# Kernel optimization log

Hardware: AMD Instinct MI355X
Metric: run time of the kernel (lower is better)

## Reference

```python
import jax, jax.numpy as jnp
import numpy as np

B, T, D, H = 8, 128, 768, 768  # batch, num tokens (actual==virtual), dim, hidden_dim
LN_EPS = 1e-5


def setup_inputs() -> dict:
    key = jax.random.key(0)
    ks = jax.random.split(key, 7)
    s1 = 1.0 / np.sqrt(D)  # torch nn.Linear init scale (uniform bound)
    s2 = 1.0 / np.sqrt(H)
    return {
        "x": jax.random.normal(ks[0], (B, T, D), dtype=jnp.float32),
        "gamma": jnp.ones((T, D), dtype=jnp.float32),
        "beta": jnp.zeros((T, D), dtype=jnp.float32),
        "W1": jax.random.uniform(ks[1], (T, D, H), minval=-s1, maxval=s1, dtype=jnp.float32),
        "b1": jax.random.uniform(ks[2], (T, H), minval=-s1, maxval=s1, dtype=jnp.float32),
        "W2": jax.random.uniform(ks[3], (T, H, D), minval=-s2, maxval=s2, dtype=jnp.float32),
        "b2": jax.random.uniform(ks[4], (T, D), minval=-s2, maxval=s2, dtype=jnp.float32),
    }


def reference(x, gamma, beta, W1, b1, W2, b2):
    # Per-token FeedForward with distinct weights per token position, fully batched
    # (equivalent to the per-token Python loop in the torch module, with
    # num_actual_tokens == num_virtual_tokens so no repeat happens).
    mu = jnp.mean(x, axis=-1, keepdims=True)
    var = jnp.mean(jnp.square(x - mu), axis=-1, keepdims=True)
    xn = (x - mu) * jax.lax.rsqrt(var + LN_EPS)
    xn = xn * gamma[None] + beta[None]                      # [B,T,D]
    h = jnp.einsum('btd,tdh->bth', xn, W1) + b1[None]       # [B,T,H]
    h = jax.nn.gelu(h, approximate=False)                   # torch nn.GELU default (erf)
    out = jnp.einsum('bth,thd->btd', h, W2) + b2[None]      # [B,T,D]
    return out + x  # residual
```

## Files before the change

kernel.cpp:

```cpp
#include <hip/hip_runtime.h>
#include <math.h>

#define TB 8
#define TT 128
#define TD 768
#define TH 768
#define LN_EPS 1e-5f

__global__ __launch_bounds__(256) void ff1_kernel(
    const float* __restrict__ x,
    const float* __restrict__ gamma,
    const float* __restrict__ beta,
    const float* __restrict__ W1,
    const float* __restrict__ b1,
    float* __restrict__ hbuf) {
  __shared__ float st[TB][TD];
  __shared__ float red[4][8][128];
  const int tid = threadIdx.x;
  const int w = tid >> 6, lane = tid & 63;
  const int half = lane >> 5, l32 = lane & 31;
  const int t = blockIdx.x / 6, slice = blockIdx.x % 6;

  {
    const int b = w * 2 + half;
    const float* xr = x + ((size_t)b * TT + t) * TD;
    float4 v[6];
    float s = 0.f, ss = 0.f;
#pragma unroll
    for (int i = 0; i < 6; ++i) {
      v[i] = *(const float4*)(xr + i * 128 + l32 * 4);
      s += v[i].x + v[i].y + v[i].z + v[i].w;
      ss += v[i].x * v[i].x + v[i].y * v[i].y + v[i].z * v[i].z + v[i].w * v[i].w;
    }
#pragma unroll
    for (int off = 16; off; off >>= 1) {
      s  += __shfl_xor(s, off, 64);
      ss += __shfl_xor(ss, off, 64);
    }
    const float mu   = s * (1.f / TD);
    const float var  = ss * (1.f / TD) - mu * mu;
    const float rstd = rsqrtf(var + LN_EPS);
#pragma unroll
    for (int i = 0; i < 6; ++i) {
      const int d = i * 128 + l32 * 4;
      const float4 g  = *(const float4*)(gamma + (size_t)t * TD + d);
      const float4 be = *(const float4*)(beta  + (size_t)t * TD + d);
      float4 o;
      o.x = (v[i].x - mu) * rstd * g.x + be.x;
      o.y = (v[i].y - mu) * rstd * g.y + be.y;
      o.z = (v[i].z - mu) * rstd * g.z + be.z;
      o.w = (v[i].w - mu) * rstd * g.w + be.w;
      *(float4*)&st[b][d] = o;
    }
  }
  __syncthreads();

  const int cg = l32 * 4;
  const int c = slice * 128 + cg;
  const int r0 = w * 192 + half * 96;
  const float* wp = W1 + ((size_t)t * TD + r0) * TH + c;

  float acc[8][4];
#pragma unroll
  for (int b = 0; b < 8; ++b)
#pragma unroll
    for (int j = 0; j < 4; ++j) acc[b][j] = 0.f;

#pragma unroll 2
  for (int dd = 0; dd < 96; dd += 4) {
    float4 wv[4];
#pragma unroll
    for (int k = 0; k < 4; ++k) wv[k] = *(const float4*)(wp + k * TH);
    wp += 4 * TH;
    float4 xq[8];
#pragma unroll
    for (int b = 0; b < 8; ++b) xq[b] = *(const float4*)&st[b][r0 + dd];
#pragma unroll
    for (int k = 0; k < 4; ++k)
#pragma unroll
      for (int b = 0; b < 8; ++b) {
        const float xv = ((const float*)&xq[b])[k];
        acc[b][0] = fmaf(xv, wv[k].x, acc[b][0]);
        acc[b][1] = fmaf(xv, wv[k].y, acc[b][1]);
        acc[b][2] = fmaf(xv, wv[k].z, acc[b][2]);
        acc[b][3] = fmaf(xv, wv[k].w, acc[b][3]);
      }
  }

#pragma unroll
  for (int b = 0; b < 8; ++b)
#pragma unroll
    for (int j = 0; j < 4; ++j)
      acc[b][j] += __shfl_xor(acc[b][j], 32, 64);

  if (lane < 32) {
#pragma unroll
    for (int b = 0; b < 8; ++b)
      *(float4*)&red[w][b][cg] =
          make_float4(acc[b][0], acc[b][1], acc[b][2], acc[b][3]);
  }
  __syncthreads();

  {
    const int b = tid >> 5;
    const int colq = (tid & 31) * 4;
    const int cc = slice * 128 + colq;
    const float4 bias = *(const float4*)(b1 + (size_t)t * TH + cc);
    float4 o;
    float* po = (float*)&o;
    const float* pb = (const float*)&bias;
#pragma unroll
    for (int k = 0; k < 4; ++k) {
      float vv = red[0][b][colq + k] + red[1][b][colq + k] +
                 red[2][b][colq + k] + red[3][b][colq + k] + pb[k];
      po[k] = 0.5f * vv * (1.f + erff(vv * 0.7071067811865476f));
    }
    *(float4*)(hbuf + ((size_t)t * TB + b) * TH + cc) = o;
  }
}

__global__ __launch_bounds__(256) void ff2_kernel(
    const float* __restrict__ hbuf,
    const float* __restrict__ W2,
    const float* __restrict__ b2,
    const float* __restrict__ x,
    float* __restrict__ out) {
  __shared__ float st[TB][TH];
  __shared__ float red[4][8][128];
  const int tid = threadIdx.x;
  const int w = tid >> 6, lane = tid & 63;
  const int half = lane >> 5, l32 = lane & 31;
  const int t = blockIdx.x / 6, slice = blockIdx.x % 6;

  {
    const float4* src = (const float4*)(hbuf + (size_t)t * TB * TH);
    float4* dst = (float4*)&st[0][0];
#pragma unroll
    for (int i = 0; i < 6; ++i) dst[tid + i * 256] = src[tid + i * 256];
  }
  __syncthreads();

  const int cg = l32 * 4;
  const int c = slice * 128 + cg;
  const int r0 = w * 192 + half * 96;
  const float* wp = W2 + ((size_t)t * TH + r0) * TD + c;

  float acc[8][4];
#pragma unroll
  for (int b = 0; b < 8; ++b)
#pragma unroll
    for (int j = 0; j < 4; ++j) acc[b][j] = 0.f;

#pragma unroll 2
  for (int dd = 0; dd < 96; dd += 4) {
    float4 wv[4];
#pragma unroll
    for (int k = 0; k < 4; ++k) wv[k] = *(const float4*)(wp + k * TD);
    wp += 4 * TD;
    float4 hq[8];
#pragma unroll
    for (int b = 0; b < 8; ++b) hq[b] = *(const float4*)&st[b][r0 + dd];
#pragma unroll
    for (int k = 0; k < 4; ++k)
#pragma unroll
      for (int b = 0; b < 8; ++b) {
        const float hv = ((const float*)&hq[b])[k];
        acc[b][0] = fmaf(hv, wv[k].x, acc[b][0]);
        acc[b][1] = fmaf(hv, wv[k].y, acc[b][1]);
        acc[b][2] = fmaf(hv, wv[k].z, acc[b][2]);
        acc[b][3] = fmaf(hv, wv[k].w, acc[b][3]);
      }
  }

#pragma unroll
  for (int b = 0; b < 8; ++b)
#pragma unroll
    for (int j = 0; j < 4; ++j)
      acc[b][j] += __shfl_xor(acc[b][j], 32, 64);

  if (lane < 32) {
#pragma unroll
    for (int b = 0; b < 8; ++b)
      *(float4*)&red[w][b][cg] =
          make_float4(acc[b][0], acc[b][1], acc[b][2], acc[b][3]);
  }
  __syncthreads();

  {
    const int b = tid >> 5;
    const int colq = (tid & 31) * 4;
    const int cc = slice * 128 + colq;
    const size_t off = ((size_t)b * TT + t) * TD + cc;
    const float4 bias = *(const float4*)(b2 + (size_t)t * TD + cc);
    const float4 xres = *(const float4*)(x + off);
    float4 o;
    float* po = (float*)&o;
    const float* pb = (const float*)&bias;
    const float* px = (const float*)&xres;
#pragma unroll
    for (int k = 0; k < 4; ++k)
      po[k] = red[0][b][colq + k] + red[1][b][colq + k] +
              red[2][b][colq + k] + red[3][b][colq + k] + pb[k] + px[k];
    *(float4*)(out + off) = o;
  }
}

extern "C" void kernel_launch(void* const* d_in, const int* in_sizes, int n_in,
                              void* d_out, int out_size, void* d_ws, size_t ws_size,
                              hipStream_t stream) {
  const float* x     = (const float*)d_in[0];
  const float* gamma = (const float*)d_in[1];
  const float* beta  = (const float*)d_in[2];
  const float* W1    = (const float*)d_in[3];
  const float* b1    = (const float*)d_in[4];
  const float* W2    = (const float*)d_in[5];
  const float* b2    = (const float*)d_in[6];
  float* out = (float*)d_out;

  float* hbuf = (float*)d_ws;

  ff1_kernel<<<TT * 6, 256, 0, stream>>>(x, gamma, beta, W1, b1, hbuf);
  ff2_kernel<<<TT * 6, 256, 0, stream>>>(hbuf, W2, b2, x, out);
}
```

Measured before the change: 115.6 us.

## Fuse both FFN stages into one kernel with per-token atomic handoff

Merges the two GEMM kernels into one. The six slice blocks of a token write their GELU outputs to a workspace buffer, bump a per-token atomic counter, then spin until all six have arrived before running the second GEMM. The first rows of W1 and then W2 are prefetched into registers early, so the load latency overlaps with layernorm and with the counter wait. This removes one kernel launch boundary and the tail gap between stages. It adds a memset launch, spin-wait cost and register pressure, and relies on all 768 blocks being co-resident (launch bounds 256,3) to avoid deadlock.

```diff
diff --git a/kernel.cpp b/kernel.cpp
--- a/kernel.cpp
+++ b/kernel.cpp
@@ -7,19 +7,49 @@
 #define TH 768
 #define LN_EPS 1e-5f
 
-__global__ __launch_bounds__(256) void ff1_kernel(
+#define BODY4(WV, ROW)                                                \
+  {                                                                   \
+    float4 xq[8];                                                     \
+    _Pragma("unroll") for (int b = 0; b < 8; ++b)                     \
+        xq[b] = *(const float4*)&st[b][(ROW)];                        \
+    _Pragma("unroll") for (int k = 0; k < 4; ++k) {                   \
+      _Pragma("unroll") for (int b = 0; b < 8; ++b) {                 \
+        const float xv = ((const float*)&xq[b])[k];                   \
+        acc[b][0] = fmaf(xv, (WV)[k].x, acc[b][0]);                   \
+        acc[b][1] = fmaf(xv, (WV)[k].y, acc[b][1]);                   \
+        acc[b][2] = fmaf(xv, (WV)[k].z, acc[b][2]);                   \
+        acc[b][3] = fmaf(xv, (WV)[k].w, acc[b][3]);                   \
+      }                                                               \
+    }                                                                 \
+  }
+
+__global__ __launch_bounds__(256, 3) void fused_ff_kernel(
     const float* __restrict__ x,
     const float* __restrict__ gamma,
     const float* __restrict__ beta,
     const float* __restrict__ W1,
     const float* __restrict__ b1,
-    float* __restrict__ hbuf) {
+    const float* __restrict__ W2,
+    const float* __restrict__ b2,
+    float* __restrict__ hbuf,
+    int* __restrict__ cnt,
+    float* __restrict__ outp) {
   __shared__ float st[TB][TD];
   __shared__ float red[4][8][128];
   const int tid = threadIdx.x;
   const int w = tid >> 6, lane = tid & 63;
   const int half = lane >> 5, l32 = lane & 31;
   const int t = blockIdx.x / 6, slice = blockIdx.x % 6;
+  const int cg = l32 * 4;
+  const int c = slice * 128 + cg;
+  const int r0 = w * 192 + half * 96;
+
+  const float* wp1 = W1 + ((size_t)t * TD + r0) * TH + c;
+  float4 pA[4], pB[4];
+#pragma unroll
+  for (int k = 0; k < 4; ++k) pA[k] = *(const float4*)(wp1 + k * TH);
+#pragma unroll
+  for (int k = 0; k < 4; ++k) pB[k] = *(const float4*)(wp1 + (4 + k) * TH);
 
   {
     const int b = w * 2 + half;
@@ -30,7 +60,8 @@
     for (int i = 0; i < 6; ++i) {
       v[i] = *(const float4*)(xr + i * 128 + l32 * 4);
       s += v[i].x + v[i].y + v[i].z + v[i].w;
-      ss += v[i].x * v[i].x + v[i].y * v[i].y + v[i].z * v[i].z + v[i].w * v[i].w;
+      ss += v[i].x * v[i].x + v[i].y * v[i].y + v[i].z * v[i].z +
+            v[i].w * v[i].w;
     }
 #pragma unroll
     for (int off = 16; off; off >>= 1) {
@@ -55,36 +86,24 @@
   }
   __syncthreads();
 
-  const int cg = l32 * 4;
-  const int c = slice * 128 + cg;
-  const int r0 = w * 192 + half * 96;
-  const float* wp = W1 + ((size_t)t * TD + r0) * TH + c;
-
   float acc[8][4];
 #pragma unroll
   for (int b = 0; b < 8; ++b)
 #pragma unroll
     for (int j = 0; j < 4; ++j) acc[b][j] = 0.f;
 
+  BODY4(pA, r0);
+  BODY4(pB, r0 + 4);
+  {
+    const float* wp = wp1 + 8 * TH;
 #pragma unroll 2
-  for (int dd = 0; dd < 96; dd += 4) {
-    float4 wv[4];
-#pragma unroll
-    for (int k = 0; k < 4; ++k) wv[k] = *(const float4*)(wp + k * TH);
-    wp += 4 * TH;
-    float4 xq[8];
-#pragma unroll
-    for (int b = 0; b < 8; ++b) xq[b] = *(const float4*)&st[b][r0 + dd];
-#pragma unroll
-    for (int k = 0; k < 4; ++k)
-#pragma unroll
-      for (int b = 0; b < 8; ++b) {
-        const float xv = ((const float*)&xq[b])[k];
-        acc[b][0] = fmaf(xv, wv[k].x, acc[b][0]);
-        acc[b][1] = fmaf(xv, wv[k].y, acc[b][1]);
-        acc[b][2] = fmaf(xv, wv[k].z, acc[b][2]);
-        acc[b][3] = fmaf(xv, wv[k].w, acc[b][3]);
-      }
+    for (int dd = 8; dd < 96; dd += 4) {
+      float4 wv[4];
+#pragma unroll
+      for (int k = 0; k < 4; ++k) wv[k] = *(const float4*)(wp + k * TH);
+      wp += 4 * TH;
+      BODY4(wv, r0 + dd);
+    }
   }
 
 #pragma unroll
@@ -92,7 +111,6 @@
 #pragma unroll
     for (int j = 0; j < 4; ++j)
       acc[b][j] += __shfl_xor(acc[b][j], 32, 64);
-
   if (lane < 32) {
 #pragma unroll
     for (int b = 0; b < 8; ++b)
@@ -117,20 +135,24 @@
     }
     *(float4*)(hbuf + ((size_t)t * TB + b) * TH + cc) = o;
   }
-}
-
-__global__ __launch_bounds__(256) void ff2_kernel(
-    const float* __restrict__ hbuf,
-    const float* __restrict__ W2,
-    const float* __restrict__ b2,
-    const float* __restrict__ x,
-    float* __restrict__ out) {
-  __shared__ float st[TB][TH];
-  __shared__ float red[4][8][128];
-  const int tid = threadIdx.x;
-  const int w = tid >> 6, lane = tid & 63;
-  const int half = lane >> 5, l32 = lane & 31;
-  const int t = blockIdx.x / 6, slice = blockIdx.x % 6;
+  __syncthreads();
+
+  if (tid == 0)
+    __hip_atomic_fetch_add(cnt + t, 1, __ATOMIC_RELEASE,
+                           __HIP_MEMORY_SCOPE_AGENT);
+
+  const float* wp2 = W2 + ((size_t)t * TH + r0) * TD + c;
+#pragma unroll
+  for (int k = 0; k < 4; ++k) pA[k] = *(const float4*)(wp2 + k * TD);
+#pragma unroll
+  for (int k = 0; k < 4; ++k) pB[k] = *(const float4*)(wp2 + (4 + k) * TD);
+
+  if (tid == 0) {
+    while (__hip_atomic_load(cnt + t, __ATOMIC_ACQUIRE,
+                             __HIP_MEMORY_SCOPE_AGENT) < 6)
+      __builtin_amdgcn_s_sleep(2);
+  }
+  __syncthreads();
 
   {
     const float4* src = (const float4*)(hbuf + (size_t)t * TB * TH);
@@ -140,36 +162,23 @@
   }
   __syncthreads();
 
-  const int cg = l32 * 4;
-  const int c = slice * 128 + cg;
-  const int r0 = w * 192 + half * 96;
-  const float* wp = W2 + ((size_t)t * TH + r0) * TD + c;
-
-  float acc[8][4];
 #pragma unroll
   for (int b = 0; b < 8; ++b)
 #pragma unroll
     for (int j = 0; j < 4; ++j) acc[b][j] = 0.f;
 
+  BODY4(pA, r0);
+  BODY4(pB, r0 + 4);
+  {
+    const float* wp = wp2 + 8 * TD;
 #pragma unroll 2
-  for (int dd = 0; dd < 96; dd += 4) {
-    float4 wv[4];
-#pragma unroll
-    for (int k = 0; k < 4; ++k) wv[k] = *(const float4*)(wp + k * TD);
-    wp += 4 * TD;
-    float4 hq[8];
-#pragma unroll
-    for (int b = 0; b < 8; ++b) hq[b] = *(const float4*)&st[b][r0 + dd];
-#pragma unroll
-    for (int k = 0; k < 4; ++k)
-#pragma unroll
-      for (int b = 0; b < 8; ++b) {
-        const float hv = ((const float*)&hq[b])[k];
-        acc[b][0] = fmaf(hv, wv[k].x, acc[b][0]);
-        acc[b][1] = fmaf(hv, wv[k].y, acc[b][1]);
-        acc[b][2] = fmaf(hv, wv[k].z, acc[b][2]);
-        acc[b][3] = fmaf(hv, wv[k].w, acc[b][3]);
-      }
+    for (int dd = 8; dd < 96; dd += 4) {
+      float4 wv[4];
+#pragma unroll
+      for (int k = 0; k < 4; ++k) wv[k] = *(const float4*)(wp + k * TD);
+      wp += 4 * TD;
+      BODY4(wv, r0 + dd);
+    }
   }
 
 #pragma unroll
@@ -177,7 +186,6 @@
 #pragma unroll
     for (int j = 0; j < 4; ++j)
       acc[b][j] += __shfl_xor(acc[b][j], 32, 64);
-
   if (lane < 32) {
 #pragma unroll
     for (int b = 0; b < 8; ++b)
@@ -201,7 +209,7 @@
     for (int k = 0; k < 4; ++k)
       po[k] = red[0][b][colq + k] + red[1][b][colq + k] +
               red[2][b][colq + k] + red[3][b][colq + k] + pb[k] + px[k];
-    *(float4*)(out + off) = o;
+    *(float4*)(outp + off) = o;
   }
 }
 
@@ -218,7 +226,9 @@
   float* out = (float*)d_out;
 
   float* hbuf = (float*)d_ws;
-
-  ff1_kernel<<<TT * 6, 256, 0, stream>>>(x, gamma, beta, W1, b1, hbuf);
-  ff2_kernel<<<TT * 6, 256, 0, stream>>>(hbuf, W2, b2, x, out);
+  int* cnt = (int*)((char*)d_ws + (size_t)TT * TB * TH * sizeof(float));
+
+  hipMemsetAsync(cnt, 0, TT * sizeof(int), stream);
+  fused_ff_kernel<<<TT * 6, 256, 0, stream>>>(x, gamma, beta, W1, b1, W2, b2,
+                                              hbuf, cnt, out);
 }
```

Result: slower. 164.4 us (+42.2%).

## Split into LN, row-chunked double-buffered GEMMs with partial sums, and reduce kernel

Applied to the files above, without the earlier changes.

Replaces the two fused kernels with four: a standalone LayerNorm kernel, two GEMM kernels where each block owns a 128-row K-chunk of the per-token weight matrix and streams it through double-buffered shared memory, and a final reduction kernel. Each GEMM block writes partial sums for all 768 outputs, and the next stage sums the six partials, then adds bias and applies GELU or the residual. The aim is fully coalesced contiguous weight streaming with register-prefetch overlap. In exchange it adds more launches and significant workspace traffic for partials, and falls back to the old path when the workspace is too small.

```diff
diff --git a/kernel.cpp b/kernel.cpp
--- a/kernel.cpp
+++ b/kernel.cpp
@@ -7,25 +7,214 @@
 #define TH 768
 #define LN_EPS 1e-5f
 
-__global__ __launch_bounds__(256) void ff1_kernel(
+
+__global__ __launch_bounds__(256) void ln_kernel(
     const float* __restrict__ x,
     const float* __restrict__ gamma,
     const float* __restrict__ beta,
-    const float* __restrict__ W1,
-    const float* __restrict__ b1,
-    float* __restrict__ hbuf) {
+    float* __restrict__ xn) {
+  const int w = threadIdx.x >> 6, lane = threadIdx.x & 63;
+  const int r = blockIdx.x * 4 + w;
+  const int t = r & (TT - 1);
+  const int b = r >> 7;
+  const float* xr = x + (size_t)r * TD;
+
+  float v[12];
+  float s = 0.f, ss = 0.f;
+#pragma unroll
+  for (int i = 0; i < 3; ++i) {
+    float4 f = *(const float4*)(xr + i * 256 + lane * 4);
+    v[i * 4 + 0] = f.x; v[i * 4 + 1] = f.y;
+    v[i * 4 + 2] = f.z; v[i * 4 + 3] = f.w;
+    s += f.x + f.y + f.z + f.w;
+    ss += f.x * f.x + f.y * f.y + f.z * f.z + f.w * f.w;
+  }
+#pragma unroll
+  for (int off = 32; off; off >>= 1) {
+    s  += __shfl_down(s, off, 64);
+    ss += __shfl_down(ss, off, 64);
+  }
+  s = __shfl(s, 0, 64); ss = __shfl(ss, 0, 64);
+  const float mu   = s * (1.f / TD);
+  const float var  = ss * (1.f / TD) - mu * mu;
+  const float rstd = rsqrtf(var + LN_EPS);
+
+#pragma unroll
+  for (int i = 0; i < 3; ++i) {
+    const int d = i * 256 + lane * 4;
+    float4 g  = *(const float4*)(gamma + (size_t)t * TD + d);
+    float4 be = *(const float4*)(beta  + (size_t)t * TD + d);
+    float4 o;
+    o.x = (v[i * 4 + 0] - mu) * rstd * g.x + be.x;
+    o.y = (v[i * 4 + 1] - mu) * rstd * g.y + be.y;
+    o.z = (v[i * 4 + 2] - mu) * rstd * g.z + be.z;
+    o.w = (v[i * 4 + 3] - mu) * rstd * g.w + be.w;
+    *(float4*)(xn + ((size_t)t * TB + b) * TD + d) = o;
+  }
+}
+
+template <int IS_G2>
+__global__ __launch_bounds__(256, 3) void gemm_kernel(
+    const float* __restrict__ act_src,
+    const float* __restrict__ W,
+    const float* __restrict__ bias,
+    float* __restrict__ pout) {
+  __shared__ float wt[2][8][768];
+  __shared__ float as[TB][128];
+  const int tid = threadIdx.x;
+  const int t = blockIdx.x / 6, chunk = blockIdx.x % 6;
+  const int c0 = tid * 3;
+
+  const float* wbase = W + ((size_t)t * 768 + chunk * 128) * 768;
+
+  float4 rstage[6];
+#pragma unroll
+  for (int k = 0; k < 6; ++k)
+    rstage[k] = *(const float4*)(wbase + (tid + k * 256) * 4);
+
+  {
+    const int b = tid >> 5, q = (tid & 31) * 4;
+    if (IS_G2) {
+      float4 sum;
+      {
+        const float* p = act_src + ((size_t)(t * 6 + 0) * TB + b) * 768 +
+                         chunk * 128 + q;
+        sum = *(const float4*)p;
+      }
+#pragma unroll
+      for (int c = 1; c < 6; ++c) {
+        const float* p = act_src + ((size_t)(t * 6 + c) * TB + b) * 768 +
+                         chunk * 128 + q;
+        const float4 v = *(const float4*)p;
+        sum.x += v.x; sum.y += v.y; sum.z += v.z; sum.w += v.w;
+      }
+      const float4 bv = *(const float4*)(bias + (size_t)t * TH + chunk * 128 + q);
+      float4 o;
+      o.x = sum.x + bv.x; o.y = sum.y + bv.y;
+      o.z = sum.z + bv.z; o.w = sum.w + bv.w;
+      float* po = (float*)&o;
+#pragma unroll
+      for (int k = 0; k < 4; ++k)
+        po[k] = 0.5f * po[k] * (1.f + erff(po[k] * 0.7071067811865476f));
+      *(float4*)&as[b][q] = o;
+    } else {
+      *(float4*)&as[b][q] =
+          *(const float4*)(act_src + ((size_t)t * TB + b) * TD + chunk * 128 + q);
+    }
+  }
+
+#pragma unroll
+  for (int k = 0; k < 6; ++k)
+    *(float4*)&wt[0][0][(tid + k * 256) * 4] = rstage[k];
+  __syncthreads();
+
+  float acc[8][3];
+#pragma unroll
+  for (int b = 0; b < 8; ++b)
+#pragma unroll
+    for (int j = 0; j < 3; ++j) acc[b][j] = 0.f;
+
+#pragma unroll 1
+  for (int tile = 0; tile < 16; ++tile) {
+    const int buf = tile & 1;
+    if (tile < 15) {
+      const float* src = wbase + (size_t)(tile + 1) * 8 * 768;
+#pragma unroll
+      for (int k = 0; k < 6; ++k)
+        rstage[k] = *(const float4*)(src + (tid + k * 256) * 4);
+    }
+    float wr[8][3];
+#pragma unroll
+    for (int r = 0; r < 8; ++r)
+#pragma unroll
+      for (int j = 0; j < 3; ++j) wr[r][j] = wt[buf][r][c0 + j];
+#pragma unroll
+    for (int b = 0; b < 8; ++b) {
+      float xa[8];
+      *(float4*)&xa[0] = *(const float4*)&as[b][tile * 8];
+      *(float4*)&xa[4] = *(const float4*)&as[b][tile * 8 + 4];
+#pragma unroll
+      for (int r = 0; r < 8; ++r) {
+        acc[b][0] = fmaf(xa[r], wr[r][0], acc[b][0]);
+        acc[b][1] = fmaf(xa[r], wr[r][1], acc[b][1]);
+        acc[b][2] = fmaf(xa[r], wr[r][2], acc[b][2]);
+      }
+    }
+    if (tile < 15) {
+#pragma unroll
+      for (int k = 0; k < 6; ++k)
+        *(float4*)&wt[buf ^ 1][0][(tid + k * 256) * 4] = rstage[k];
+    }
+    __syncthreads();
+  }
+
+  float* ob = &wt[0][0][0];
+#pragma unroll
+  for (int b = 0; b < 8; ++b)
+#pragma unroll
+    for (int j = 0; j < 3; ++j) ob[b * 768 + c0 + j] = acc[b][j];
+  __syncthreads();
+  {
+    float* dst = pout + (size_t)(t * 6 + chunk) * TB * 768;
+#pragma unroll
+    for (int k = 0; k < 6; ++k)
+      *(float4*)(dst + (tid + k * 256) * 4) =
+          *(const float4*)(ob + (tid + k * 256) * 4);
+  }
+}
+
+__global__ __launch_bounds__(256) void k4_kernel(
+    const float* __restrict__ p2,
+    const float* __restrict__ b2,
+    const float* __restrict__ x,
+    float* __restrict__ out) {
+  const int f = (blockIdx.x * 256 + threadIdx.x) * 4;
+  const int b = f / (TT * TD);
+  const int r = f % (TT * TD);
+  const int t = r / TD, d = r % TD;
+  float4 acc = *(const float4*)(b2 + r);
+  const float4 xv = *(const float4*)(x + f);
+  acc.x += xv.x; acc.y += xv.y; acc.z += xv.z; acc.w += xv.w;
+#pragma unroll
+  for (int c = 0; c < 6; ++c) {
+    const float4 v =
+        *(const float4*)(p2 + ((size_t)(t * 6 + c) * TB + b) * TD + d);
+    acc.x += v.x; acc.y += v.y; acc.z += v.z; acc.w += v.w;
+  }
+  *(float4*)(out + f) = acc;
+}
+
+#define BODY4(WV, ROW)                                                \
+  {                                                                   \
+    float4 xq[8];                                                     \
+    _Pragma("unroll") for (int b = 0; b < 8; ++b)                     \
+        xq[b] = *(const float4*)&st[b][(ROW)];                        \
+    _Pragma("unroll") for (int k = 0; k < 4; ++k) {                   \
+      _Pragma("unroll") for (int b = 0; b < 8; ++b) {                 \
+        const float xv = ((const float*)&xq[b])[k];                   \
+        acc[b][0] = fmaf(xv, (WV)[k].x, acc[b][0]);                   \
+        acc[b][1] = fmaf(xv, (WV)[k].y, acc[b][1]);                   \
+        acc[b][2] = fmaf(xv, (WV)[k].z, acc[b][2]);                   \
+        acc[b][3] = fmaf(xv, (WV)[k].w, acc[b][3]);                   \
+      }                                                               \
+    }                                                                 \
+  }
+
+__global__ __launch_bounds__(256) void ff1_fb(
+    const float* __restrict__ x, const float* __restrict__ gamma,
+    const float* __restrict__ beta, const float* __restrict__ W1,
+    const float* __restrict__ b1, float* __restrict__ hbuf) {
   __shared__ float st[TB][TD];
   __shared__ float red[4][8][128];
   const int tid = threadIdx.x;
   const int w = tid >> 6, lane = tid & 63;
   const int half = lane >> 5, l32 = lane & 31;
   const int t = blockIdx.x / 6, slice = blockIdx.x % 6;
-
+  const int cg = l32 * 4, c = slice * 128 + cg, r0 = w * 192 + half * 96;
   {
     const int b = w * 2 + half;
     const float* xr = x + ((size_t)b * TT + t) * TD;
-    float4 v[6];
-    float s = 0.f, ss = 0.f;
+    float4 v[6]; float s = 0.f, ss = 0.f;
 #pragma unroll
     for (int i = 0; i < 6; ++i) {
       v[i] = *(const float4*)(xr + i * 128 + l32 * 4);
@@ -33,97 +222,64 @@
       ss += v[i].x * v[i].x + v[i].y * v[i].y + v[i].z * v[i].z + v[i].w * v[i].w;
     }
 #pragma unroll
-    for (int off = 16; off; off >>= 1) {
-      s  += __shfl_xor(s, off, 64);
-      ss += __shfl_xor(ss, off, 64);
-    }
-    const float mu   = s * (1.f / TD);
-    const float var  = ss * (1.f / TD) - mu * mu;
+    for (int off = 16; off; off >>= 1) { s += __shfl_xor(s, off, 64); ss += __shfl_xor(ss, off, 64); }
+    const float mu = s * (1.f / TD), var = ss * (1.f / TD) - mu * mu;
     const float rstd = rsqrtf(var + LN_EPS);
 #pragma unroll
     for (int i = 0; i < 6; ++i) {
       const int d = i * 128 + l32 * 4;
-      const float4 g  = *(const float4*)(gamma + (size_t)t * TD + d);
-      const float4 be = *(const float4*)(beta  + (size_t)t * TD + d);
+      const float4 g = *(const float4*)(gamma + (size_t)t * TD + d);
+      const float4 be = *(const float4*)(beta + (size_t)t * TD + d);
       float4 o;
-      o.x = (v[i].x - mu) * rstd * g.x + be.x;
-      o.y = (v[i].y - mu) * rstd * g.y + be.y;
-      o.z = (v[i].z - mu) * rstd * g.z + be.z;
-      o.w = (v[i].w - mu) * rstd * g.w + be.w;
+      o.x = (v[i].x - mu) * rstd * g.x + be.x; o.y = (v[i].y - mu) * rstd * g.y + be.y;
+      o.z = (v[i].z - mu) * rstd * g.z + be.z; o.w = (v[i].w - mu) * rstd * g.w + be.w;
       *(float4*)&st[b][d] = o;
     }
   }
   __syncthreads();
-
-  const int cg = l32 * 4;
-  const int c = slice * 128 + cg;
-  const int r0 = w * 192 + half * 96;
-  const float* wp = W1 + ((size_t)t * TD + r0) * TH + c;
-
   float acc[8][4];
 #pragma unroll
   for (int b = 0; b < 8; ++b)
 #pragma unroll
     for (int j = 0; j < 4; ++j) acc[b][j] = 0.f;
-
+  {
+    const float* wp = W1 + ((size_t)t * TD + r0) * TH + c;
 #pragma unroll 2
-  for (int dd = 0; dd < 96; dd += 4) {
-    float4 wv[4];
-#pragma unroll
-    for (int k = 0; k < 4; ++k) wv[k] = *(const float4*)(wp + k * TH);
-    wp += 4 * TH;
-    float4 xq[8];
-#pragma unroll
-    for (int b = 0; b < 8; ++b) xq[b] = *(const float4*)&st[b][r0 + dd];
-#pragma unroll
-    for (int k = 0; k < 4; ++k)
-#pragma unroll
-      for (int b = 0; b < 8; ++b) {
-        const float xv = ((const float*)&xq[b])[k];
-        acc[b][0] = fmaf(xv, wv[k].x, acc[b][0]);
-        acc[b][1] = fmaf(xv, wv[k].y, acc[b][1]);
-        acc[b][2] = fmaf(xv, wv[k].z, acc[b][2]);
-        acc[b][3] = fmaf(xv, wv[k].w, acc[b][3]);
-      }
-  }
-
-#pragma unroll
-  for (int b = 0; b < 8; ++b)
-#pragma unroll
-    for (int j = 0; j < 4; ++j)
-      acc[b][j] += __shfl_xor(acc[b][j], 32, 64);
-
+    for (int dd = 0; dd < 96; dd += 4) {
+      float4 wv[4];
+#pragma unroll
+      for (int k = 0; k < 4; ++k) wv[k] = *(const float4*)(wp + k * TH);
+      wp += 4 * TH;
+      BODY4(wv, r0 + dd);
+    }
+  }
+#pragma unroll
+  for (int b = 0; b < 8; ++b)
+#pragma unroll
+    for (int j = 0; j < 4; ++j) acc[b][j] += __shfl_xor(acc[b][j], 32, 64);
   if (lane < 32) {
 #pragma unroll
     for (int b = 0; b < 8; ++b)
-      *(float4*)&red[w][b][cg] =
-          make_float4(acc[b][0], acc[b][1], acc[b][2], acc[b][3]);
-  }
-  __syncthreads();
-
-  {
-    const int b = tid >> 5;
-    const int colq = (tid & 31) * 4;
-    const int cc = slice * 128 + colq;
+      *(float4*)&red[w][b][cg] = make_float4(acc[b][0], acc[b][1], acc[b][2], acc[b][3]);
+  }
+  __syncthreads();
+  {
+    const int b = tid >> 5, colq = (tid & 31) * 4, cc = slice * 128 + colq;
     const float4 bias = *(const float4*)(b1 + (size_t)t * TH + cc);
-    float4 o;
-    float* po = (float*)&o;
-    const float* pb = (const float*)&bias;
+    float4 o; float* po = (float*)&o; const float* pb = (const float*)&bias;
 #pragma unroll
     for (int k = 0; k < 4; ++k) {
-      float vv = red[0][b][colq + k] + red[1][b][colq + k] +
-                 red[2][b][colq + k] + red[3][b][colq + k] + pb[k];
+      float vv = red[0][b][colq + k] + red[1][b][colq + k] + red[2][b][colq + k] +
+                 red[3][b][colq + k] + pb[k];
       po[k] = 0.5f * vv * (1.f + erff(vv * 0.7071067811865476f));
     }
     *(float4*)(hbuf + ((size_t)t * TB + b) * TH + cc) = o;
   }
 }
 
-__global__ __launch_bounds__(256) void ff2_kernel(
-    const float* __restrict__ hbuf,
-    const float* __restrict__ W2,
-    const float* __restrict__ b2,
-    const float* __restrict__ x,
+__global__ __launch_bounds__(256) void ff2_fb(
+    const float* __restrict__ hbuf, const float* __restrict__ W2,
+    const float* __restrict__ b2, const float* __restrict__ x,
     float* __restrict__ out) {
   __shared__ float st[TB][TH];
   __shared__ float red[4][8][128];
@@ -131,7 +287,7 @@
   const int w = tid >> 6, lane = tid & 63;
   const int half = lane >> 5, l32 = lane & 31;
   const int t = blockIdx.x / 6, slice = blockIdx.x % 6;
-
+  const int cg = l32 * 4, c = slice * 128 + cg, r0 = w * 192 + half * 96;
   {
     const float4* src = (const float4*)(hbuf + (size_t)t * TB * TH);
     float4* dst = (float4*)&st[0][0];
@@ -139,68 +295,43 @@
     for (int i = 0; i < 6; ++i) dst[tid + i * 256] = src[tid + i * 256];
   }
   __syncthreads();
-
-  const int cg = l32 * 4;
-  const int c = slice * 128 + cg;
-  const int r0 = w * 192 + half * 96;
-  const float* wp = W2 + ((size_t)t * TH + r0) * TD + c;
-
   float acc[8][4];
 #pragma unroll
   for (int b = 0; b < 8; ++b)
 #pragma unroll
     for (int j = 0; j < 4; ++j) acc[b][j] = 0.f;
-
+  {
+    const float* wp = W2 + ((size_t)t * TH + r0) * TD + c;
 #pragma unroll 2
-  for (int dd = 0; dd < 96; dd += 4) {
-    float4 wv[4];
-#pragma unroll
-    for (int k = 0; k < 4; ++k) wv[k] = *(const float4*)(wp + k * TD);
-    wp += 4 * TD;
-    float4 hq[8];
-#pragma unroll
-    for (int b = 0; b < 8; ++b) hq[b] = *(const float4*)&st[b][r0 + dd];
-#pragma unroll
-    for (int k = 0; k < 4; ++k)
-#pragma unroll
-      for (int b = 0; b < 8; ++b) {
-        const float hv = ((const float*)&hq[b])[k];
-        acc[b][0] = fmaf(hv, wv[k].x, acc[b][0]);
-        acc[b][1] = fmaf(hv, wv[k].y, acc[b][1]);
-        acc[b][2] = fmaf(hv, wv[k].z, acc[b][2]);
-        acc[b][3] = fmaf(hv, wv[k].w, acc[b][3]);
-      }
-  }
-
-#pragma unroll
-  for (int b = 0; b < 8; ++b)
-#pragma unroll
-    for (int j = 0; j < 4; ++j)
-      acc[b][j] += __shfl_xor(acc[b][j], 32, 64);
-
+    for (int dd = 0; dd < 96; dd += 4) {
+      float4 wv[4];
+#pragma unroll
+      for (int k = 0; k < 4; ++k) wv[k] = *(const float4*)(wp + k * TD);
+      wp += 4 * TD;
+      BODY4(wv, r0 + dd);
+    }
+  }
+#pragma unroll
+  for (int b = 0; b < 8; ++b)
+#pragma unroll
+    for (int j = 0; j < 4; ++j) acc[b][j] += __shfl_xor(acc[b][j], 32, 64);
   if (lane < 32) {
 #pragma unroll
     for (int b = 0; b < 8; ++b)
-      *(float4*)&red[w][b][cg] =
-          make_float4(acc[b][0], acc[b][1], acc[b][2], acc[b][3]);
-  }
-  __syncthreads();
-
-  {
-    const int b = tid >> 5;
-    const int colq = (tid & 31) * 4;
-    const int cc = slice * 128 + colq;
+      *(float4*)&red[w][b][cg] = make_float4(acc[b][0], acc[b][1], acc[b][2], acc[b][3]);
+  }
+  __syncthreads();
+  {
+    const int b = tid >> 5, colq = (tid & 31) * 4, cc = slice * 128 + colq;
     const size_t off = ((size_t)b * TT + t) * TD + cc;
     const float4 bias = *(const float4*)(b2 + (size_t)t * TD + cc);
     const float4 xres = *(const float4*)(x + off);
-    float4 o;
-    float* po = (float*)&o;
-    const float* pb = (const float*)&bias;
-    const float* px = (const float*)&xres;
+    float4 o; float* po = (float*)&o;
+    const float* pb = (const float*)&bias; const float* px = (const float*)&xres;
 #pragma unroll
     for (int k = 0; k < 4; ++k)
-      po[k] = red[0][b][colq + k] + red[1][b][colq + k] +
-              red[2][b][colq + k] + red[3][b][colq + k] + pb[k] + px[k];
+      po[k] = red[0][b][colq + k] + red[1][b][colq + k] + red[2][b][colq + k] +
+              red[3][b][colq + k] + pb[k] + px[k];
     *(float4*)(out + off) = o;
   }
 }
@@ -217,8 +348,21 @@
   const float* b2    = (const float*)d_in[6];
   float* out = (float*)d_out;
 
-  float* hbuf = (float*)d_ws;
-
-  ff1_kernel<<<TT * 6, 256, 0, stream>>>(x, gamma, beta, W1, b1, hbuf);
-  ff2_kernel<<<TT * 6, 256, 0, stream>>>(hbuf, W2, b2, x, out);
-}
+  const size_t n_xn = (size_t)TT * TB * TD;
+  const size_t n_p  = (size_t)TT * 6 * TB * 768;
+  const size_t need = (n_xn + 2 * n_p) * sizeof(float);
+
+  if (ws_size >= need) {
+    float* xn = (float*)d_ws;
+    float* p1 = xn + n_xn;
+    float* p2 = p1 + n_p;
+    ln_kernel<<<256, 256, 0, stream>>>(x, gamma, beta, xn);
+    gemm_kernel<0><<<TT * 6, 256, 0, stream>>>(xn, W1, nullptr, p1);
+    gemm_kernel<1><<<TT * 6, 256, 0, stream>>>(p1, W2, b1, p2);
+    k4_kernel<<<(TB * TT * TD) / (256 * 4), 256, 0, stream>>>(p2, b2, x, out);
+  } else {
+    float* hbuf = (float*)d_ws;
+    ff1_fb<<<TT * 6, 256, 0, stream>>>(x, gamma, beta, W1, b1, hbuf);
+    ff2_fb<<<TT * 6, 256, 0, stream>>>(hbuf, W2, b2, x, out);
+  }
+}
```

Result: slower. 245.9 us (+112.8%).
